# Performance work log

Hardware: AMD Instinct MI355X
Metric: run time of the kernel (lower is better)

Reference implementation:

```python
import jax, jax.numpy as jnp
import numpy as np

B, C, NH, WS, NC = 8, 768, 12, 8, 1
HD = C // NH  # 64


def _window_partition(t, H, W):
    # t: [B, NH, H*W, HD] -> [B*nw, NH, WS*WS, HD]
    t = t.reshape(B, NH, H // WS, WS, W // WS, WS, HD)
    t = t.transpose(0, 2, 4, 1, 3, 5, 6)
    return t.reshape(-1, NH, WS * WS, HD)


def _window_reverse(t, H, W):
    # t: [B*nw, WS*WS, C] -> [B, H*W, C]
    t = t.reshape(B, H // WS, W // WS, WS, WS, C)
    t = t.transpose(0, 1, 3, 2, 4, 5)
    return t.reshape(B, H * W, C)


def setup_inputs() -> dict:
    key = jax.random.key(0)
    ks = jax.random.split(key, 8)
    H = W = 64
    N = NC + H * W
    x = jax.random.normal(ks[0], (B, N, C), jnp.float32)
    # per-token 0/1 mask broadcast over channels (matches mask@mask^T semantics)
    tok = (jax.random.uniform(ks[1], (B, H * W, 1)) > 0.2).astype(jnp.float32)
    mask = jnp.broadcast_to(tok, (B, H * W, C))
    global_mask = (jax.random.uniform(ks[2], (B, NH, NC, H * W)) > 0.5).astype(jnp.float32)
    s = 0.02
    qkv_w = jax.random.normal(ks[3], (C, 3 * C), jnp.float32) * s
    kv_global_w = jax.random.normal(ks[4], (C, 2 * C), jnp.float32) * s
    proj_w = jax.random.normal(ks[5], (C, C), jnp.float32) * s
    proj_b = jnp.zeros((C,), jnp.float32)
    return {"x": x, "mask": mask, "global_mask": global_mask, "qkv_w": qkv_w,
            "kv_global_w": kv_global_w, "proj_w": proj_w, "proj_b": proj_b,
            "H": H, "W": W}


def reference(x, mask, global_mask, qkv_w, kv_global_w, proj_w, proj_b, H, W):
    scale = HD ** -0.5
    HW = H * W
    NEG = -10000.0

    # qkv projection (no bias), split heads: [B, NH, N, HD]
    qkv = (x @ qkv_w).reshape(B, NC + HW, 3, NH, HD).transpose(2, 0, 3, 1, 4)
    q, k, v = qkv[0], qkv[1], qkv[2]
    m = mask.reshape(B, HW, NH, HD).transpose(0, 2, 1, 3)  # [B, NH, HW, HD]

    q_img, k_img, v_img = q[:, :, NC:], k[:, :, NC:], v[:, :, NC:]
    q_cls = q[:, :, :NC]

    # ---- local windowed attention ----
    qw = _window_partition(q_img, H, W)
    kw = _window_partition(k_img, H, W)
    vw = _window_partition(v_img, H, W)
    mw = _window_partition(m, H, W)
    am = (mw @ jnp.swapaxes(mw, -2, -1)) / HD          # [B*nw, NH, ws2, ws2]
    attn = (qw @ jnp.swapaxes(kw, -2, -1)) * scale
    attn = jnp.where(am == 0, NEG, attn)
    attn = jax.nn.softmax(attn, axis=-1)
    xl = (attn @ vw).transpose(0, 2, 1, 3).reshape(-1, WS * WS, C)
    x_img = _window_reverse(xl, H, W)                  # [B, HW, C]

    # ---- global aggregation (global tokens attend to image tokens) ----
    key_cov = jnp.sum(m, axis=-1) / HD                 # ones @ m^T / hd -> [B, NH, HW]
    am_g = key_cov[:, :, None, :] * global_mask        # [B, NH, NC, HW]
    attn_g = (q_cls @ jnp.swapaxes(k_img, -2, -1)) * scale
    attn_g = jnp.where(am_g == 0, NEG, attn_g)
    attn_g = jax.nn.softmax(attn_g, axis=-1)
    x_cls = (attn_g @ v_img).transpose(0, 2, 1, 3).reshape(B, NC, C)

    # kv_global projection of aggregated global tokens
    kv_g = (x_cls @ kv_global_w).reshape(B, NC, 2, NH, HD).transpose(2, 0, 3, 1, 4)
    k_cls, v_cls = kv_g[0], kv_g[1]                    # [B, NH, NC, HD]

    # ---- global broadcast (image tokens attend to global tokens) ----
    am_b = (jnp.sum(m, axis=-1) / HD)[..., None]       # m @ ones^T / hd -> [B, NH, HW, 1]
    am_b = jnp.broadcast_to(am_b, (B, NH, HW, NC))
    attn_b = (q_img @ jnp.swapaxes(k_cls, -2, -1)) * scale
    attn_b = jnp.where(am_b == 0, NEG, attn_b)
    attn_b = jax.nn.softmax(attn_b, axis=-1)
    xb = (attn_b @ v_cls).transpose(0, 2, 1, 3).reshape(B, HW, C)

    x_img = x_img + xb
    out = jnp.concatenate([x_cls, x_img], axis=1) @ proj_w + proj_b
    return out
```

## Files before the change

### kernel.cpp

```cpp
#include <hip/hip_runtime.h>

#define B_    8
#define C_    768
#define NH_   12
#define HW_   4096
#define NTOK  4097
#define MTOT  32776
#define NEGV  (-10000.0f)
#define NSPLIT 16

typedef __bf16 bf16x8 __attribute__((ext_vector_type(8)));
typedef float  f32x4  __attribute__((ext_vector_type(4)));
typedef unsigned short us8 __attribute__((ext_vector_type(8)));

#define GLB(p) ((const __attribute__((address_space(1))) void*)(p))
#define LDS(p) ((__attribute__((address_space(3))) void*)(p))

__device__ __forceinline__ float us2f(unsigned short u) {
    unsigned int v = ((unsigned int)u) << 16;
    float f; __builtin_memcpy(&f, &v, 4);
    return f;
}
__device__ __forceinline__ unsigned short f2us(float f) {
    unsigned int v; __builtin_memcpy(&v, &f, 4);
    v += 0x7FFFu + ((v >> 16) & 1u);
    return (unsigned short)(v >> 16);
}

__global__ __launch_bounds__(256) void detect_dtype(
    const unsigned int* __restrict__ xw, int* __restrict__ flag)
{
    __shared__ int s[256];
    int t = threadIdx.x, cnt = 0;
    for (int i = t; i < 4096; i += 256) {
        unsigned e = (xw[i] >> 23) & 0xFFu;
        cnt += (e >= 64u && e <= 191u) ? 1 : 0;
    }
    s[t] = cnt; __syncthreads();
    for (int k = 128; k > 0; k >>= 1) { if (t < k) s[t] += s[t + k]; __syncthreads(); }
    if (t == 0) *flag = (s[0] > 2048) ? 1 : 0;
}

__global__ __launch_bounds__(256) void transpose_w(
    const unsigned short* __restrict__ s16, const float* __restrict__ s32,
    const int* __restrict__ flagp, unsigned short* __restrict__ dst,
    int Kd, int Nd)
{
    int o = blockIdx.x * 256 + threadIdx.x;
    if (o >= Kd * Nd) return;
    int n = o / Kd, k = o % Kd;
    dst[o] = (*flagp) ? f2us(s32[(size_t)k * Nd + n]) : s16[(size_t)k * Nd + n];
}

__global__ __launch_bounds__(256) void gemm_bt(
    const unsigned short* __restrict__ A16, const float* __restrict__ A32,
    const int* __restrict__ aflagp,
    const unsigned short* __restrict__ BT,
    const unsigned short* __restrict__ bias16, const float* __restrict__ bias32,
    const int* __restrict__ bflagp,
    void* __restrict__ Cout, const int* __restrict__ oflagp,
    int M, int Nd, int K, long arow0)
{
    __shared__ __align__(16) unsigned short As[128 * 64];
    __shared__ __align__(16) unsigned short Bs[128 * 64];

    const int fa = aflagp ? *aflagp : 0;
    const int fb = bflagp ? *bflagp : 0;
    const int fo = oflagp ? *oflagp : 0;

    const int t    = threadIdx.x;

    const int nbx = gridDim.x;
    const int nwg = nbx * gridDim.y;
    const int lin = blockIdx.y * nbx + blockIdx.x;
    const int q   = nwg >> 3, r = nwg & 7;
    const int xcd = lin & 7, loc = lin >> 3;
    const int wg  = (xcd < r ? xcd * (q + 1) : r * (q + 1) + (xcd - r) * q) + loc;
    const int m0  = (wg / nbx) * 128;
    const int n0  = (wg % nbx) * 128;

    const int wave = t >> 6;
    const int lane = t & 63;
    const int wm   = (wave >> 1) * 64;
    const int wn   = (wave & 1) * 64;
    const int frow = lane & 15;
    const int lsl  = lane >> 4;

    f32x4 acc[4][4];
#pragma unroll
    for (int i = 0; i < 4; ++i)
#pragma unroll
        for (int j = 0; j < 4; ++j) acc[i][j] = (f32x4)0.0f;

    const int tr   = t >> 3;
    const int srcc = (((t & 7) ^ (tr & 7)) * 8);

    const float* aF[4];
    const unsigned short* aP[4];
    const unsigned short* bP[4];
#pragma unroll
    for (int it = 0; it < 4; ++it) {
        int ga = m0 + tr + it * 32; if (ga >= M)  ga = M - 1;
        int gb = n0 + tr + it * 32; if (gb >= Nd) gb = Nd - 1;
        aP[it] = A16 + (size_t)(arow0 + ga) * K + srcc;
        aF[it] = A32 + (size_t)(arow0 + ga) * K + srcc;
        bP[it] = BT  + (size_t)gb * K + srcc;
    }

    for (int k0 = 0; k0 < K; k0 += 64) {
        if (fa) {
#pragma unroll
            for (int it = 0; it < 4; ++it) {
                unsigned short tmp[8];
                const float* p = aF[it] + k0;
#pragma unroll
                for (int e = 0; e < 8; ++e) tmp[e] = f2us(p[e]);
                *reinterpret_cast<us8*>(&As[it * 2048 + t * 8]) = *reinterpret_cast<us8*>(tmp);
            }
        } else {
#pragma unroll
            for (int it = 0; it < 4; ++it)
                __builtin_amdgcn_global_load_lds(GLB(aP[it] + k0), LDS(&As[it * 2048 + t * 8]), 16, 0, 0);
        }
#pragma unroll
        for (int it = 0; it < 4; ++it)
            __builtin_amdgcn_global_load_lds(GLB(bP[it] + k0), LDS(&Bs[it * 2048 + t * 8]), 16, 0, 0);
        __syncthreads();

#pragma unroll
        for (int kk = 0; kk < 64; kk += 32) {
            const int ksl = (kk >> 3) + lsl;
            bf16x8 af[4], bfr[4];
#pragma unroll
            for (int i = 0; i < 4; ++i) {
                int ra = wm + i * 16 + frow;
                af[i] = *reinterpret_cast<const bf16x8*>(&As[ra * 64 + ((ksl ^ (ra & 7)) << 3)]);
            }
#pragma unroll
            for (int j = 0; j < 4; ++j) {
                int rb = wn + j * 16 + frow;
                bfr[j] = *reinterpret_cast<const bf16x8*>(&Bs[rb * 64 + ((ksl ^ (rb & 7)) << 3)]);
            }
#pragma unroll
            for (int i = 0; i < 4; ++i)
#pragma unroll
                for (int j = 0; j < 4; ++j)
                    acc[i][j] = __builtin_amdgcn_mfma_f32_16x16x32_bf16(af[i], bfr[j], acc[i][j], 0, 0, 0);
        }
        __syncthreads();
    }

    const int crow = (lane >> 4) * 4;
    const int ccol = lane & 15;
    unsigned short* C16 = (unsigned short*)Cout;
    float*          C32 = (float*)Cout;
#pragma unroll
    for (int i = 0; i < 4; ++i)
#pragma unroll
        for (int j = 0; j < 4; ++j) {
            int gn = n0 + wn + j * 16 + ccol;
            float bv = 0.0f;
            if (bias16) bv = fb ? bias32[gn] : us2f(bias16[gn]);
#pragma unroll
            for (int r2 = 0; r2 < 4; ++r2) {
                int gm = m0 + wm + i * 16 + crow + r2;
                if (gm < M) {
                    float v = acc[i][j][r2] + bv;
                    if (fo) C32[(size_t)gm * Nd + gn] = v;
                    else    C16[(size_t)gm * Nd + gn] = f2us(v);
                }
            }
        }
}

#define LSTR 40

__global__ __launch_bounds__(256) void gemm_univ(
    const unsigned short* __restrict__ A16, const float* __restrict__ A32,
    const int* __restrict__ aflagp,
    const unsigned short* __restrict__ B16, const float* __restrict__ B32,
    const int* __restrict__ bflagp, int btmode,
    const unsigned short* __restrict__ bias16, const float* __restrict__ bias32,
    void* __restrict__ Cout, const int* __restrict__ oflagp,
    int M, int Nd, int K, long arow0)
{
    __shared__ __align__(16) unsigned short As[128 * LSTR];
    __shared__ __align__(16) unsigned short Bs[128 * LSTR];

    const int fa = aflagp ? *aflagp : 0;
    const int fb = bflagp ? *bflagp : 0;
    const int fo = oflagp ? *oflagp : 0;

    const int t    = threadIdx.x;
    const int m0   = blockIdx.y * 128;
    const int n0   = blockIdx.x * 128;
    const int wave = t >> 6;
    const int lane = t & 63;
    const int wm   = (wave >> 1) * 64;
    const int wn   = (wave & 1) * 64;
    const int frow = lane & 15;
    const int koff = (lane >> 4) * 8;

    f32x4 acc[4][4];
#pragma unroll
    for (int i = 0; i < 4; ++i)
#pragma unroll
        for (int j = 0; j < 4; ++j) acc[i][j] = (f32x4)0.0f;

    const int sr = t >> 2;
    const int sc = (t & 3) * 8;

    for (int k0 = 0; k0 < K; k0 += 32) {
#pragma unroll
        for (int it = 0; it < 2; ++it) {
            int r = sr + it * 64;
            int gl = m0 + r; if (gl >= M) gl = M - 1;
            size_t grow = (size_t)(arow0 + gl);
            if (fa) {
                const float* p = &A32[grow * K + k0 + sc];
                unsigned short tmp[8];
#pragma unroll
                for (int e = 0; e < 8; ++e) tmp[e] = f2us(p[e]);
                *reinterpret_cast<us8*>(&As[r * LSTR + sc]) = *reinterpret_cast<us8*>(tmp);
            } else {
                *reinterpret_cast<bf16x8*>(&As[r * LSTR + sc]) =
                    *reinterpret_cast<const bf16x8*>(&A16[grow * K + k0 + sc]);
            }
        }
        if (btmode == 0) {
#pragma unroll
            for (int it = 0; it < 2; ++it) {
                int r = sr + it * 64;
                int gn = n0 + r; if (gn >= Nd) gn = Nd - 1;
                *reinterpret_cast<bf16x8*>(&Bs[r * LSTR + sc]) =
                    *reinterpret_cast<const bf16x8*>(&B16[(size_t)gn * K + k0 + sc]);
            }
        } else {
            const int kr = t >> 3;
            const int nc = (t & 7) * 16;
            if (fb) {
                const float* p = &B32[(size_t)(k0 + kr) * Nd + n0 + nc];
#pragma unroll
                for (int e = 0; e < 16; ++e) Bs[(nc + e) * LSTR + kr] = f2us(p[e]);
            } else {
                const unsigned short* p = &B16[(size_t)(k0 + kr) * Nd + n0 + nc];
#pragma unroll
                for (int e = 0; e < 16; ++e) Bs[(nc + e) * LSTR + kr] = p[e];
            }
        }
        __syncthreads();

        bf16x8 af[4], bfr[4];
#pragma unroll
        for (int i = 0; i < 4; ++i)
            af[i] = *reinterpret_cast<const bf16x8*>(&As[(wm + i * 16 + frow) * LSTR + koff]);
#pragma unroll
        for (int j = 0; j < 4; ++j)
            bfr[j] = *reinterpret_cast<const bf16x8*>(&Bs[(wn + j * 16 + frow) * LSTR + koff]);
#pragma unroll
        for (int i = 0; i < 4; ++i)
#pragma unroll
            for (int j = 0; j < 4; ++j)
                acc[i][j] = __builtin_amdgcn_mfma_f32_16x16x32_bf16(af[i], bfr[j], acc[i][j], 0, 0, 0);
        __syncthreads();
    }

    const int crow = (lane >> 4) * 4;
    const int ccol = lane & 15;
    unsigned short* C16 = (unsigned short*)Cout;
    float*          C32 = (float*)Cout;
#pragma unroll
    for (int i = 0; i < 4; ++i)
#pragma unroll
        for (int j = 0; j < 4; ++j) {
            int gn = n0 + wn + j * 16 + ccol;
            float bv = 0.0f;
            if (bias16) bv = fb ? bias32[gn] : us2f(bias16[gn]);
#pragma unroll
            for (int r = 0; r < 4; ++r) {
                int gm = m0 + wm + i * 16 + crow + r;
                if (gm < M) {
                    float v = acc[i][j][r] + bv;
                    if (fo) C32[(size_t)gm * Nd + gn] = v;
                    else    C16[(size_t)gm * Nd + gn] = f2us(v);
                }
            }
        }
}

#define AST 72
#define SST 65

__global__ __launch_bounds__(256) void win_attn(
    const unsigned short* __restrict__ qkv2,
    const unsigned short* __restrict__ m16, const float* __restrict__ m32,
    const int* __restrict__ flagp,
    unsigned short* __restrict__ xcat, int b0)
{
    __shared__ __align__(16) unsigned short qs[64 * AST];
    __shared__ __align__(16) unsigned short ks[64 * AST];
    __shared__ __align__(16) unsigned short vsT[64 * AST];
    __shared__ float S[64 * SST];
    __shared__ float tok[64];

    const int w  = blockIdx.x;
    const int h  = blockIdx.y;
    const int bb = blockIdx.z;
    const int b  = b0 + bb;
    const int hb = w >> 3, wb = w & 7;
    const int t  = threadIdx.x;
    const int f  = *flagp;
    const unsigned short* qkvb = qkv2 + (size_t)bb * NTOK * 2304;

#define POS(i) ((hb * 8 + ((i) >> 3)) * 64 + wb * 8 + ((i) & 7))

#pragma unroll
    for (int it = 0; it < 2; ++it) {
        int i = (t >> 3) + it * 32;
        int d = (t & 7) * 8;
        size_t row = (size_t)(1 + POS(i)) * 2304;
        bf16x8 qv = *reinterpret_cast<const bf16x8*>(&qkvb[row + 0    + h * 64 + d]);
        bf16x8 kv = *reinterpret_cast<const bf16x8*>(&qkvb[row + 768  + h * 64 + d]);
        us8    vv = *reinterpret_cast<const us8*>  (&qkvb[row + 1536 + h * 64 + d]);
        *reinterpret_cast<bf16x8*>(&qs[i * AST + d]) = qv;
        *reinterpret_cast<bf16x8*>(&ks[i * AST + d]) = kv;
#pragma unroll
        for (int e = 0; e < 8; ++e) vsT[(d + e) * AST + i] = vv[e];
    }
    if (t < 64) {
        size_t mi = ((size_t)b * HW_ + POS(t)) * C_;
        tok[t] = f ? m32[mi] : us2f(m16[mi]);
    }
    __syncthreads();

    const int wave = t >> 6;
    const int lane = t & 63;
    const int wm   = (wave >> 1) * 32;
    const int wn   = (wave & 1) * 32;
    const int frow = lane & 15;
    const int koff = (lane >> 4) * 8;
    const int crow = (lane >> 4) * 4;
    const int ccol = lane & 15;

    {
        f32x4 acc[2][2];
#pragma unroll
        for (int i = 0; i < 2; ++i)
#pragma unroll
            for (int j = 0; j < 2; ++j) acc[i][j] = (f32x4)0.0f;
#pragma unroll
        for (int kk = 0; kk < 64; kk += 32) {
            bf16x8 af[2], bfr[2];
#pragma unroll
            for (int i = 0; i < 2; ++i)
                af[i] = *reinterpret_cast<const bf16x8*>(&qs[(wm + i * 16 + frow) * AST + kk + koff]);
#pragma unroll
            for (int j = 0; j < 2; ++j)
                bfr[j] = *reinterpret_cast<const bf16x8*>(&ks[(wn + j * 16 + frow) * AST + kk + koff]);
#pragma unroll
            for (int i = 0; i < 2; ++i)
#pragma unroll
                for (int j = 0; j < 2; ++j)
                    acc[i][j] = __builtin_amdgcn_mfma_f32_16x16x32_bf16(af[i], bfr[j], acc[i][j], 0, 0, 0);
        }
#pragma unroll
        for (int i = 0; i < 2; ++i)
#pragma unroll
            for (int j = 0; j < 2; ++j)
#pragma unroll
                for (int r = 0; r < 4; ++r)
                    S[(wm + i * 16 + crow + r) * SST + wn + j * 16 + ccol] = acc[i][j][r];
    }
    __syncthreads();

    {
        const int r = t >> 2;
        const int q = t & 3;
        const float tr = tok[r];
        float sv[16];
        float mx = -1e30f;
#pragma unroll
        for (int e = 0; e < 16; ++e) {
            int c = q * 16 + e;
            float s = S[r * SST + c] * 0.125f;
            if (tr * tok[c] == 0.0f) s = NEGV;
            sv[e] = s;
            mx = fmaxf(mx, s);
        }
        mx = fmaxf(mx, __shfl_xor(mx, 1));
        mx = fmaxf(mx, __shfl_xor(mx, 2));
        float sum = 0.f;
#pragma unroll
        for (int e = 0; e < 16; ++e) { sv[e] = __expf(sv[e] - mx); sum += sv[e]; }
        sum += __shfl_xor(sum, 1);
        sum += __shfl_xor(sum, 2);
        const float inv = 1.0f / sum;
        unsigned short* ps = qs;
        us8 o0, o1;
#pragma unroll
        for (int e = 0; e < 8; ++e) { o0[e] = f2us(sv[e] * inv); o1[e] = f2us(sv[8 + e] * inv); }
        *reinterpret_cast<us8*>(&ps[r * AST + q * 16])     = o0;
        *reinterpret_cast<us8*>(&ps[r * AST + q * 16 + 8]) = o1;
    }
    __syncthreads();

    {
        const unsigned short* ps = qs;
        f32x4 acc[2][2];
#pragma unroll
        for (int i = 0; i < 2; ++i)
#pragma unroll
            for (int j = 0; j < 2; ++j) acc[i][j] = (f32x4)0.0f;
#pragma unroll
        for (int kk = 0; kk < 64; kk += 32) {
            bf16x8 af[2], bfr[2];
#pragma unroll
            for (int i = 0; i < 2; ++i)
                af[i] = *reinterpret_cast<const bf16x8*>(&ps[(wm + i * 16 + frow) * AST + kk + koff]);
#pragma unroll
            for (int j = 0; j < 2; ++j)
                bfr[j] = *reinterpret_cast<const bf16x8*>(&vsT[(wn + j * 16 + frow) * AST + kk + koff]);
#pragma unroll
            for (int i = 0; i < 2; ++i)
#pragma unroll
                for (int j = 0; j < 2; ++j)
                    acc[i][j] = __builtin_amdgcn_mfma_f32_16x16x32_bf16(af[i], bfr[j], acc[i][j], 0, 0, 0);
        }
#pragma unroll
        for (int i = 0; i < 2; ++i)
#pragma unroll
            for (int j = 0; j < 2; ++j)
#pragma unroll
                for (int r = 0; r < 4; ++r) {
                    int qrow = wm + i * 16 + crow + r;
                    int dcol = wn + j * 16 + ccol;
                    xcat[(size_t)(b * NTOK + 1 + POS(qrow)) * C_ + h * 64 + dcol] =
                        f2us(acc[i][j][r]);
                }
    }
#undef POS
}

__global__ __launch_bounds__(256) void cls_part(
    const unsigned short* __restrict__ qkv2,
    const unsigned short* __restrict__ m16, const float* __restrict__ m32,
    const unsigned short* __restrict__ g16, const float* __restrict__ g32,
    const int* __restrict__ flagp,
    float* __restrict__ part,
    int b0)
{
    __shared__ float q[64];
    __shared__ float e[256];
    __shared__ float red[256];
    __shared__ float osum[4][64];
    __shared__ float Mv, Sv;

    const int h  = blockIdx.x;
    const int sp = blockIdx.y;
    const int bb = blockIdx.z;
    const int b  = b0 + bb;
    const int t  = threadIdx.x;
    const int f  = *flagp;
    const unsigned short* qkvb = qkv2 + (size_t)bb * NTOK * 2304;

    if (t < 64) q[t] = us2f(qkvb[h * 64 + t]);
    __syncthreads();

    const int j = sp * 256 + t;
    const unsigned short* krow = &qkvb[(size_t)(1 + j) * 2304 + 768 + h * 64];
    float s = 0.f;
#pragma unroll
    for (int dd = 0; dd < 8; ++dd) {
        us8 kv8 = *reinterpret_cast<const us8*>(&krow[dd * 8]);
#pragma unroll
        for (int ee = 0; ee < 8; ++ee) s += q[dd * 8 + ee] * us2f(kv8[ee]);
    }
    s *= 0.125f;
    {
        size_t mi = ((size_t)b * HW_ + j) * C_;
        size_t gi = ((size_t)b * NH_ + h) * HW_ + j;
        float tokj = f ? m32[mi] : us2f(m16[mi]);
        float gmj  = f ? g32[gi] : us2f(g16[gi]);
        if (tokj * gmj == 0.0f) s = NEGV;
    }

    red[t] = s; __syncthreads();
    for (int k2 = 128; k2 > 0; k2 >>= 1) { if (t < k2) red[t] = fmaxf(red[t], red[t + k2]); __syncthreads(); }
    const float m = red[0]; __syncthreads();

    float ev = __expf(s - m);
    e[t] = ev; red[t] = ev; __syncthreads();
    for (int k2 = 128; k2 > 0; k2 >>= 1) { if (t < k2) red[t] += red[t + k2]; __syncthreads(); }
    if (t == 0) { Mv = m; Sv = red[0]; }

    const int wv = t >> 6, l = t & 63;
    float accv = 0.f;
    const unsigned short* vbase =
        &qkvb[(size_t)(1 + sp * 256 + wv * 64) * 2304 + 1536 + h * 64 + l];
    for (int kk = 0; kk < 64; ++kk)
        accv += e[wv * 64 + kk] * us2f(vbase[(size_t)kk * 2304]);
    osum[wv][l] = accv;
    __syncthreads();

    const size_t pi = ((size_t)(b * NH_ + h) * NSPLIT + sp) * 68;
    if (t < 64)
        part[pi + t] = osum[0][t] + osum[1][t] + osum[2][t] + osum[3][t];
    if (t == 64 + 0) part[pi + 64] = Mv;
    if (t == 64 + 1) part[pi + 65] = Sv;
}

__global__ __launch_bounds__(64) void cls_reduce(
    const float* __restrict__ part, unsigned short* __restrict__ xcat)
{
    const int h = blockIdx.x, b = blockIdx.y, t = threadIdx.x;
    const float* pb = &part[((size_t)(b * NH_ + h) * NSPLIT) * 68];
    float gm = -1e30f;
    for (int i = 0; i < NSPLIT; ++i) gm = fmaxf(gm, pb[i * 68 + 64]);
    float S = 0.f, acc = 0.f;
    for (int i = 0; i < NSPLIT; ++i) {
        float w = __expf(pb[i * 68 + 64] - gm);
        S   += pb[i * 68 + 65] * w;
        acc += pb[i * 68 + t]  * w;
    }
    xcat[(size_t)(b * NTOK) * C_ + h * 64 + t] = f2us(acc / S);
}

__global__ __launch_bounds__(256) void add_vcls(
    const unsigned short* __restrict__ xcat, unsigned short* __restrict__ xcatc,
    const unsigned short* __restrict__ kv16, const float* __restrict__ kv32,
    const int* __restrict__ flagp)
{
    __shared__ float xr[768];
    __shared__ float psum[4][64];
    __shared__ float vc[64];

    const int blk = blockIdx.x;
    const int rsp = blockIdx.y;
    const int b   = blk / 12;
    const int c0  = (blk % 12) * 64;
    const int t   = threadIdx.x;
    const int f   = *flagp;

    for (int it = 0; it < 3; ++it) {
        int k = t + it * 256;
        xr[k] = us2f(xcat[(size_t)(b * NTOK) * C_ + k]);
    }
    __syncthreads();

    const int cc = t & 63, kq = t >> 6;
    float p = 0.f;
    for (int k = kq * 192; k < kq * 192 + 192; ++k) {
        size_t wi = (size_t)k * 1536 + 768 + c0 + cc;
        p += xr[k] * (f ? kv32[wi] : us2f(kv16[wi]));
    }
    psum[kq][cc] = p;
    __syncthreads();
    if (t < 64) vc[t] = psum[0][t] + psum[1][t] + psum[2][t] + psum[3][t];
    __syncthreads();

    const int ch8  = (t & 7) * 8;
    const int rsub = t >> 3;
    for (int it = 0; it < 32; ++it) {
        int row = rsp * 1024 + it * 32 + rsub;
        size_t off = (size_t)(b * NTOK + 1 + row) * C_ + c0 + ch8;
        us8 vv = *reinterpret_cast<const us8*>(&xcat[off]);
#pragma unroll
        for (int e2 = 0; e2 < 8; ++e2)
            vv[e2] = f2us(us2f(vv[e2]) + vc[ch8 + e2]);
        *reinterpret_cast<us8*>(&xcatc[off]) = vv;
    }
    if (rsp == 0 && t < 64)
        xcatc[(size_t)(b * NTOK) * C_ + c0 + t] = xcat[(size_t)(b * NTOK) * C_ + c0 + t];
}

extern "C" void kernel_launch(void* const* d_in, const int* in_sizes, int n_in,
                              void* d_out, int out_size, void* d_ws, size_t ws_size,
                              hipStream_t stream)
{
    const unsigned short* x16  = (const unsigned short*)d_in[0];
    const float*          x32  = (const float*)d_in[0];
    const unsigned short* m16  = (const unsigned short*)d_in[1];
    const float*          m32  = (const float*)d_in[1];
    const unsigned short* g16  = (const unsigned short*)d_in[2];
    const float*          g32  = (const float*)d_in[2];
    const unsigned short* qw16 = (const unsigned short*)d_in[3];
    const float*          qw32 = (const float*)d_in[3];
    const unsigned short* kv16 = (const unsigned short*)d_in[4];
    const float*          kv32 = (const float*)d_in[4];
    const unsigned short* pw16 = (const unsigned short*)d_in[5];
    const float*          pw32 = (const float*)d_in[5];
    const unsigned short* pb16 = (const unsigned short*)d_in[6];
    const float*          pb32 = (const float*)d_in[6];

    char* ws = (char*)d_ws;
    int*            flag  = (int*)ws;
    unsigned short* xcatc = (unsigned short*)(ws + 128);
    unsigned short* xcat  = (unsigned short*)d_out;

    const bool fused = (ws_size >= (size_t)156168320);

    detect_dtype<<<1, 256, 0, stream>>>((const unsigned int*)d_in[0], flag);

    if (fused) {
        unsigned short* qkv_full = (unsigned short*)(ws + 128);
        unsigned short* qkv_wT   = (unsigned short*)(ws + 151031936);
        float*          part     = (float*)(ws + 154570880);
        unsigned short* pwT      = (unsigned short*)(ws + 154988672);

        transpose_w<<<(2304 * 768 + 255) / 256, 256, 0, stream>>>(
            qw16, qw32, flag, qkv_wT, 768, 2304);
        transpose_w<<<(768 * 768 + 255) / 256, 256, 0, stream>>>(
            pw16, pw32, flag, pwT, 768, 768);

        gemm_bt<<<dim3(18, 257), 256, 0, stream>>>(
            x16, x32, flag, qkv_wT,
            nullptr, nullptr, nullptr,
            qkv_full, nullptr,
            MTOT, 2304, 768, 0);
        win_attn<<<dim3(64, 12, 8), 256, 0, stream>>>(qkv_full, m16, m32, flag, xcat, 0);
        cls_part<<<dim3(12, NSPLIT, 8), 256, 0, stream>>>(
            qkv_full, m16, m32, g16, g32, flag, part, 0);

        cls_reduce<<<dim3(12, 8), 64, 0, stream>>>(part, xcat);
        add_vcls<<<dim3(96, 4), 256, 0, stream>>>(xcat, xcatc, kv16, kv32, flag);

        gemm_bt<<<dim3(6, 257), 256, 0, stream>>>(
            xcatc, nullptr, nullptr, pwT,
            pb16, pb32, flag,
            d_out, flag,
            MTOT, 768, 768, 0);
        return;
    }

    unsigned short* qkv_2b = (unsigned short*)(ws + 128);
    unsigned short* qkv_wT = (unsigned short*)(ws + 37758080);
    float*          part   = (float*)(ws + 41297024);
    unsigned short* pwT    = (unsigned short*)(ws + 50344064);
    const bool fastproj = (ws_size >= (size_t)51523712);

    transpose_w<<<(2304 * 768 + 255) / 256, 256, 0, stream>>>(
        qw16, qw32, flag, qkv_wT, 768, 2304);
    if (fastproj)
        transpose_w<<<(768 * 768 + 255) / 256, 256, 0, stream>>>(
            pw16, pw32, flag, pwT, 768, 768);

    for (int b0 = 0; b0 < B_; b0 += 2) {
        gemm_bt<<<dim3(18, 65), 256, 0, stream>>>(
            x16, x32, flag, qkv_wT,
            nullptr, nullptr, nullptr,
            qkv_2b, nullptr,
            2 * NTOK, 2304, 768, (long)b0 * NTOK);
        win_attn<<<dim3(64, 12, 2), 256, 0, stream>>>(qkv_2b, m16, m32, flag, xcat, b0);
        cls_part<<<dim3(12, NSPLIT, 2), 256, 0, stream>>>(
            qkv_2b, m16, m32, g16, g32, flag, part, b0);
    }

    cls_reduce<<<dim3(12, 8), 64, 0, stream>>>(part, xcat);
    add_vcls<<<dim3(96, 4), 256, 0, stream>>>(xcat, xcatc, kv16, kv32, flag);

    if (fastproj) {
        gemm_bt<<<dim3(6, 257), 256, 0, stream>>>(
            xcatc, nullptr, nullptr, pwT,
            pb16, pb32, flag,
            d_out, flag,
            MTOT, 768, 768, 0);
    } else {
        gemm_univ<<<dim3(6, 257), 256, 0, stream>>>(
            xcatc, nullptr, nullptr, pw16, pw32, flag, 1,
            pb16, pb32, d_out, flag,
            MTOT, 768, 768, 0);
    }
}
```

Before: 750.7 us.

## Double-buffer LDS tiles in bf16 GEMM with async global-to-LDS prefetch

```diff
diff --git a/kernel.cpp b/kernel.cpp
--- a/kernel.cpp
+++ b/kernel.cpp
@@ -61,8 +61,8 @@
     void* __restrict__ Cout, const int* __restrict__ oflagp,
     int M, int Nd, int K, long arow0)
 {
-    __shared__ __align__(16) unsigned short As[128 * 64];
-    __shared__ __align__(16) unsigned short Bs[128 * 64];
+    __shared__ __align__(16) unsigned short As[2][128 * 64];
+    __shared__ __align__(16) unsigned short Bs[2][128 * 64];
 
     const int fa = aflagp ? *aflagp : 0;
     const int fb = bflagp ? *bflagp : 0;
@@ -107,48 +107,86 @@
         bP[it] = BT  + (size_t)gb * K + srcc;
     }
 
-    for (int k0 = 0; k0 < K; k0 += 64) {
-        if (fa) {
+#define STAGE_TILE(buf, koff_)                                                              \
+    do {                                                                                    \
+        _Pragma("unroll")                                                                   \
+        for (int it = 0; it < 4; ++it) {                                                    \
+            __builtin_amdgcn_global_load_lds(GLB(aP[it] + (koff_)),                         \
+                LDS(&As[(buf)][it * 2048 + t * 8]), 16, 0, 0);                              \
+            __builtin_amdgcn_global_load_lds(GLB(bP[it] + (koff_)),                         \
+                LDS(&Bs[(buf)][it * 2048 + t * 8]), 16, 0, 0);                              \
+        }                                                                                   \
+    } while (0)
+
+#define COMPUTE_TILE(buf)                                                                   \
+    do {                                                                                    \
+        _Pragma("unroll")                                                                   \
+        for (int kk = 0; kk < 64; kk += 32) {                                               \
+            const int ksl = (kk >> 3) + lsl;                                                \
+            bf16x8 af[4], bfr[4];                                                           \
+            _Pragma("unroll")                                                               \
+            for (int i = 0; i < 4; ++i) {                                                   \
+                int ra = wm + i * 16 + frow;                                                \
+                af[i] = *reinterpret_cast<const bf16x8*>(                                   \
+                    &As[(buf)][ra * 64 + ((ksl ^ (ra & 7)) << 3)]);                         \
+            }                                                                               \
+            _Pragma("unroll")                                                               \
+            for (int j = 0; j < 4; ++j) {                                                   \
+                int rb = wn + j * 16 + frow;                                                \
+                bfr[j] = *reinterpret_cast<const bf16x8*>(                                  \
+                    &Bs[(buf)][rb * 64 + ((ksl ^ (rb & 7)) << 3)]);                         \
+            }                                                                               \
+            _Pragma("unroll")                                                               \
+            for (int i = 0; i < 4; ++i)                                                     \
+                _Pragma("unroll")                                                           \
+                for (int j = 0; j < 4; ++j)                                                 \
+                    acc[i][j] = __builtin_amdgcn_mfma_f32_16x16x32_bf16(                    \
+                        af[i], bfr[j], acc[i][j], 0, 0, 0);                                 \
+        }                                                                                   \
+    } while (0)
+
+    if (!fa) {
+        const int NT = K >> 6;
+        STAGE_TILE(0, 0);
+        STAGE_TILE(1, 64);
+        asm volatile("s_waitcnt vmcnt(8)" ::: "memory");
+        __builtin_amdgcn_s_barrier();
+
+        int cur = 0;
+        for (int kt = 0; kt < NT; ++kt) {
+            COMPUTE_TILE(cur);
+            __builtin_amdgcn_s_barrier();
+            if (kt + 2 < NT) {
+                const int nk = (kt + 2) << 6;
+                STAGE_TILE(cur, nk);
+                asm volatile("s_waitcnt vmcnt(8)" ::: "memory");
+            } else {
+                asm volatile("s_waitcnt vmcnt(0)" ::: "memory");
+            }
+            __builtin_amdgcn_s_barrier();
+            cur ^= 1;
+        }
+    } else {
+        for (int k0 = 0; k0 < K; k0 += 64) {
 #pragma unroll
             for (int it = 0; it < 4; ++it) {
                 unsigned short tmp[8];
                 const float* p = aF[it] + k0;
 #pragma unroll
                 for (int e = 0; e < 8; ++e) tmp[e] = f2us(p[e]);
-                *reinterpret_cast<us8*>(&As[it * 2048 + t * 8]) = *reinterpret_cast<us8*>(tmp);
+                *reinterpret_cast<us8*>(&As[0][it * 2048 + t * 8]) = *reinterpret_cast<us8*>(tmp);
             }
-        } else {
 #pragma unroll
             for (int it = 0; it < 4; ++it)
-                __builtin_amdgcn_global_load_lds(GLB(aP[it] + k0), LDS(&As[it * 2048 + t * 8]), 16, 0, 0);
-        }
-#pragma unroll
-        for (int it = 0; it < 4; ++it)
-            __builtin_amdgcn_global_load_lds(GLB(bP[it] + k0), LDS(&Bs[it * 2048 + t * 8]), 16, 0, 0);
-        __syncthreads();
-
-#pragma unroll
-        for (int kk = 0; kk < 64; kk += 32) {
-            const int ksl = (kk >> 3) + lsl;
-            bf16x8 af[4], bfr[4];
-#pragma unroll
-            for (int i = 0; i < 4; ++i) {
-                int ra = wm + i * 16 + frow;
-                af[i] = *reinterpret_cast<const bf16x8*>(&As[ra * 64 + ((ksl ^ (ra & 7)) << 3)]);
-            }
-#pragma unroll
-            for (int j = 0; j < 4; ++j) {
-                int rb = wn + j * 16 + frow;
-                bfr[j] = *reinterpret_cast<const bf16x8*>(&Bs[rb * 64 + ((ksl ^ (rb & 7)) << 3)]);
-            }
-#pragma unroll
-            for (int i = 0; i < 4; ++i)
-#pragma unroll
-                for (int j = 0; j < 4; ++j)
-                    acc[i][j] = __builtin_amdgcn_mfma_f32_16x16x32_bf16(af[i], bfr[j], acc[i][j], 0, 0, 0);
-        }
-        __syncthreads();
-    }
+                __builtin_amdgcn_global_load_lds(GLB(bP[it] + k0), LDS(&Bs[0][it * 2048 + t * 8]), 16, 0, 0);
+            __syncthreads();
+            COMPUTE_TILE(0);
+            __syncthreads();
+        }
+    }
+
+#undef STAGE_TILE
+#undef COMPUTE_TILE
 
     const int crow = (lane >> 4) * 4;
     const int ccol = lane & 15;
```

Result: no change. 747.2 us (-0.5%).
